# Kernel optimization log

Hardware: AMD Instinct MI355X
Metric: run time of the kernel (lower is better)

## Reference

```python
import jax, jax.numpy as jnp
import numpy as np

KERNEL_SIZE_FACTOR = 0.1
SIGMA = 3.0


def _determine_kernel_size(feature_map_size):
    size = int(feature_map_size * KERNEL_SIZE_FACTOR)
    return size if size % 2 == 1 else size + 1


def _gaussian_kernel_2d(size, sigma):
    # matches cv2.getGaussianKernel for sigma > 0: exp(-(i-c)^2/(2*sigma^2)), L1-normalized
    ax = jnp.arange(size, dtype=jnp.float32) - (size - 1) / 2.0
    k1 = jnp.exp(-(ax * ax) / (2.0 * sigma * sigma))
    k1 = k1 / jnp.sum(k1)
    return jnp.outer(k1, k1)  # [size, size]


def setup_inputs() -> dict:
    key = jax.random.key(0)
    k1, k2 = jax.random.split(key)
    feature_map = jax.random.normal(k1, (16, 64, 224, 224), dtype=jnp.float32)
    points = jax.random.uniform(k2, (16, 1024, 2), dtype=jnp.float32)
    return {"feature_map": feature_map, "points": points}


def reference(feature_map, points):
    B, C, H, W = feature_map.shape
    N = points.shape[1]
    ks = _determine_kernel_size(min(H, W))
    half = ks // 2
    kernel = _gaussian_kernel_2d(ks, SIGMA)

    # Boundary clipping in the original == scatter full kernel into a padded map, then crop.
    Hp, Wp = H + 2 * half, W + 2 * half

    x = (points[..., 0] * W).astype(jnp.int32)  # [B, N], floor of nonneg
    y = (points[..., 1] * H).astype(jnp.int32)  # [B, N]

    d = jnp.arange(ks, dtype=jnp.int32)
    # top-left corner in padded coords: (y - half) + half = y
    rows = y[:, :, None, None] + d[None, None, :, None]  # [B, N, ks, 1]
    cols = x[:, :, None, None] + d[None, None, None, :]  # [B, N, 1, ks]
    b = jnp.arange(B, dtype=jnp.int32)[:, None, None, None]
    flat_idx = ((b * Hp + rows) * Wp + cols).reshape(-1)  # [B*N*ks*ks]

    vals = jnp.broadcast_to(kernel, (B, N, ks, ks)).reshape(-1)
    sal = jnp.zeros(B * Hp * Wp, dtype=jnp.float32).at[flat_idx].add(vals)
    sal = sal.reshape(B, Hp, Wp)[:, half:half + H, half:half + W]
    return sal
```

## Files before the change

kernel.cpp:

```cpp
#include <hip/hip_runtime.h>
#include <math.h>

#define BB   16
#define HH   224
#define WW   224
#define NPTS 1024
#define KS   23
#define HALF 11
#define SIGMA2_2 18.0f

__device__ __forceinline__ void gauss_weights(float* w) {
    float s = 0.0f;
#pragma unroll
    for (int t = 0; t < KS; ++t) {
        float ax = (float)(t - HALF);
        float v = __expf(-(ax * ax) / SIGMA2_2);
        w[t] = v;
        s += v;
    }
    float inv = 1.0f / s;
#pragma unroll
    for (int t = 0; t < KS; ++t) w[t] *= inv;
}

__global__ void scatter_counts(const float* __restrict__ pts, float* __restrict__ cnt) {
    int idx = blockIdx.x * blockDim.x + threadIdx.x;
    if (idx >= BB * NPTS) return;
    int b = idx / NPTS;
    float px = pts[2 * idx + 0];
    float py = pts[2 * idx + 1];
    int x = (int)(px * (float)WW);
    int y = (int)(py * (float)HH);
    if ((unsigned)x >= WW || (unsigned)y >= HH) return;
    atomicAdd(&cnt[(b * HH + y) * WW + x], 1.0f);
}

__global__ void hconv(const float* __restrict__ cnt, float* __restrict__ tmp) {
    int idx = blockIdx.x * blockDim.x + threadIdx.x;
    if (idx >= BB * HH * WW) return;
    float w[KS];
    gauss_weights(w);
    int j = idx % WW;
    int rowbase = idx - j;
    float acc = 0.0f;
#pragma unroll
    for (int t = 0; t < KS; ++t) {
        int x = j + t - HALF;
        float v = ((unsigned)x < (unsigned)WW) ? cnt[rowbase + x] : 0.0f;
        acc = fmaf(v, w[t], acc);
    }
    tmp[idx] = acc;
}

__global__ void vconv(const float* __restrict__ tmp, float* __restrict__ out) {
    int idx = blockIdx.x * blockDim.x + threadIdx.x;
    if (idx >= BB * HH * WW) return;
    float w[KS];
    gauss_weights(w);
    int j = idx % WW;
    int rem = idx / WW;
    int i = rem % HH;
    int b = rem / HH;
    const float* base = tmp + (size_t)b * HH * WW + j;
    float acc = 0.0f;
#pragma unroll
    for (int t = 0; t < KS; ++t) {
        int y = i + t - HALF;
        float v = ((unsigned)y < (unsigned)HH) ? base[(size_t)y * WW] : 0.0f;
        acc = fmaf(v, w[t], acc);
    }
    out[idx] = acc;
}

extern "C" void kernel_launch(void* const* d_in, const int* in_sizes, int n_in,
                              void* d_out, int out_size, void* d_ws, size_t ws_size,
                              hipStream_t stream) {
    const float* pts = (const float*)d_in[1];
    float* out = (float*)d_out;

    const int PIX = BB * HH * WW;
    float* cnt = (float*)d_ws;
    float* tmp = cnt + PIX;

    hipMemsetAsync(cnt, 0, (size_t)PIX * sizeof(float), stream);

    scatter_counts<<<(BB * NPTS + 255) / 256, 256, 0, stream>>>(pts, cnt);
    hconv<<<(PIX + 255) / 256, 256, 0, stream>>>(cnt, tmp);
    vconv<<<(PIX + 255) / 256, 256, 0, stream>>>(tmp, out);
}
```

Measured before the change: 243.3 us.

## Fuse horizontal and vertical Gaussian passes into one LDS-tiled kernel

Replaces the separate horizontal and vertical convolution kernels with one kernel per (batch, 8-row tile). It loads the count rows plus halo into shared memory, does the horizontal pass into shared memory, then the vertical pass to the output. This removes the global intermediate buffer, one kernel launch, and the per-thread recomputation of the Gaussian weights, which are now computed once per block. In exchange it recomputes the horizontal pass on halo rows and runs with relatively few large-LDS blocks.

```diff
diff --git a/kernel.cpp b/kernel.cpp
--- a/kernel.cpp
+++ b/kernel.cpp
@@ -9,19 +9,9 @@
 #define HALF 11
 #define SIGMA2_2 18.0f
 
-__device__ __forceinline__ void gauss_weights(float* w) {
-    float s = 0.0f;
-#pragma unroll
-    for (int t = 0; t < KS; ++t) {
-        float ax = (float)(t - HALF);
-        float v = __expf(-(ax * ax) / SIGMA2_2);
-        w[t] = v;
-        s += v;
-    }
-    float inv = 1.0f / s;
-#pragma unroll
-    for (int t = 0; t < KS; ++t) w[t] *= inv;
-}
+#define TR   8
+#define ER   (TR + KS - 1)
+#define NTIL (HH / TR)
 
 __global__ void scatter_counts(const float* __restrict__ pts, float* __restrict__ cnt) {
     int idx = blockIdx.x * blockDim.x + threadIdx.x;
@@ -35,41 +25,69 @@
     atomicAdd(&cnt[(b * HH + y) * WW + x], 1.0f);
 }
 
-__global__ void hconv(const float* __restrict__ cnt, float* __restrict__ tmp) {
-    int idx = blockIdx.x * blockDim.x + threadIdx.x;
-    if (idx >= BB * HH * WW) return;
+__global__ __launch_bounds__(256) void fused_blur(const float* __restrict__ cnt,
+                                                  float* __restrict__ out) {
+    __shared__ float s_cnt[ER * WW];
+    __shared__ float s_h[ER * WW];
+    __shared__ float s_w[KS];
+
+    int blk = blockIdx.x;
+    int b = blk / NTIL;
+    int r0 = (blk % NTIL) * TR;
+
+    if (threadIdx.x == 0) {
+        float s = 0.0f;
+        float v[KS];
+#pragma unroll
+        for (int t = 0; t < KS; ++t) {
+            float ax = (float)(t - HALF);
+            v[t] = __expf(-(ax * ax) / SIGMA2_2);
+            s += v[t];
+        }
+        float inv = 1.0f / s;
+#pragma unroll
+        for (int t = 0; t < KS; ++t) s_w[t] = v[t] * inv;
+    }
+
+    const float* src = cnt + (size_t)b * HH * WW;
+    for (int q = threadIdx.x; q < ER * (WW / 4); q += 256) {
+        int r = q / (WW / 4);
+        int c = (q % (WW / 4)) * 4;
+        int gr = r0 - HALF + r;
+        float4 v = make_float4(0.f, 0.f, 0.f, 0.f);
+        if ((unsigned)gr < (unsigned)HH) v = *(const float4*)(src + (size_t)gr * WW + c);
+        *(float4*)(&s_cnt[r * WW + c]) = v;
+    }
+    __syncthreads();
+
     float w[KS];
-    gauss_weights(w);
-    int j = idx % WW;
-    int rowbase = idx - j;
-    float acc = 0.0f;
 #pragma unroll
-    for (int t = 0; t < KS; ++t) {
-        int x = j + t - HALF;
-        float v = ((unsigned)x < (unsigned)WW) ? cnt[rowbase + x] : 0.0f;
-        acc = fmaf(v, w[t], acc);
+    for (int t = 0; t < KS; ++t) w[t] = s_w[t];
+
+    for (int q = threadIdx.x; q < ER * WW; q += 256) {
+        int j = q % WW;
+        const float* row = &s_cnt[q - j];
+        float acc = 0.0f;
+#pragma unroll
+        for (int t = 0; t < KS; ++t) {
+            int x = j + t - HALF;
+            float v = ((unsigned)x < (unsigned)WW) ? row[x] : 0.0f;
+            acc = fmaf(v, w[t], acc);
+        }
+        s_h[q] = acc;
     }
-    tmp[idx] = acc;
-}
+    __syncthreads();
 
-__global__ void vconv(const float* __restrict__ tmp, float* __restrict__ out) {
-    int idx = blockIdx.x * blockDim.x + threadIdx.x;
-    if (idx >= BB * HH * WW) return;
-    float w[KS];
-    gauss_weights(w);
-    int j = idx % WW;
-    int rem = idx / WW;
-    int i = rem % HH;
-    int b = rem / HH;
-    const float* base = tmp + (size_t)b * HH * WW + j;
-    float acc = 0.0f;
+    float* dst = out + ((size_t)b * HH + r0) * WW;
+    for (int q = threadIdx.x; q < TR * WW; q += 256) {
+        int j = q % WW;
+        int r = q / WW;
+        float acc = 0.0f;
 #pragma unroll
-    for (int t = 0; t < KS; ++t) {
-        int y = i + t - HALF;
-        float v = ((unsigned)y < (unsigned)HH) ? base[(size_t)y * WW] : 0.0f;
-        acc = fmaf(v, w[t], acc);
+        for (int t = 0; t < KS; ++t)
+            acc = fmaf(s_h[(r + t) * WW + j], w[t], acc);
+        dst[q] = acc;
     }
-    out[idx] = acc;
 }
 
 extern "C" void kernel_launch(void* const* d_in, const int* in_sizes, int n_in,
@@ -80,11 +98,9 @@
 
     const int PIX = BB * HH * WW;
     float* cnt = (float*)d_ws;
-    float* tmp = cnt + PIX;
 
     hipMemsetAsync(cnt, 0, (size_t)PIX * sizeof(float), stream);
 
     scatter_counts<<<(BB * NPTS + 255) / 256, 256, 0, stream>>>(pts, cnt);
-    hconv<<<(PIX + 255) / 256, 256, 0, stream>>>(cnt, tmp);
-    vconv<<<(PIX + 255) / 256, 256, 0, stream>>>(tmp, out);
+    fused_blur<<<BB * NTIL, 256, 0, stream>>>(cnt, out);
 }
```

Result: slower. 250.3 us (+2.8%).
